# Kernel optimization log

Measured on AMD Instinct MI355X. Metric: run time of the kernel, lower is better.

Reference implementation:

```python
import jax, jax.numpy as jnp
import numpy as np

B, N, D_IN, E, H = 4, 512, 256, 64, 4
NEG = 1.0e9


def setup_inputs() -> dict:
    key = jax.random.key(0)
    ks = jax.random.split(key, 7)
    s = 1.0 / np.sqrt(D_IN)  # dense-init scale
    return {
        "x": jax.random.normal(ks[0], (B, N, D_IN), jnp.float32),
        "Wq": jax.random.normal(ks[1], (H, D_IN, E), jnp.float32) * s,
        "bq": jnp.zeros((H, E), jnp.float32),
        "Wk": jax.random.normal(ks[2], (H, D_IN, E), jnp.float32) * s,
        "bk": jnp.zeros((H, E), jnp.float32),
        "Wv": jax.random.normal(ks[3], (H, D_IN, E), jnp.float32) * s,
        "bv": jnp.zeros((H, E), jnp.float32),
    }


def _sdp(q, k, v):
    logits = jnp.einsum('bne,bme->bnm', q, k) / jnp.sqrt(jnp.asarray(E, q.dtype))
    return jnp.einsum('bnm,bme->bne', jax.nn.softmax(logits, axis=-1), v)


def _cosine(q, k, v):
    qn = q / jnp.linalg.norm(q, axis=-1, keepdims=True)
    kn = k / jnp.linalg.norm(k, axis=-1, keepdims=True)
    logits = jnp.einsum('bne,bme->bnm', qn, kn)
    return jnp.einsum('bnm,bme->bne', jax.nn.softmax(logits, axis=-1), v)


def _l1(q, k, v):
    # [B,N,N] L1 distances via broadcasted [B,N,N,E] diff, as in the original
    d = jnp.sum(jnp.abs(q[:, :, None, :] - k[:, None, :, :]), axis=-1)
    return jnp.einsum('bnm,bme->bne', jax.nn.softmax(-d, axis=-1), v)


def _l2(q, k, v):
    d = jnp.sqrt(jnp.sum(jnp.square(q[:, :, None, :] - k[:, None, :, :]), axis=-1))
    return jnp.einsum('bnm,bme->bne', jax.nn.softmax(-d, axis=-1), v)


_HEAD_FNS = (_sdp, _cosine, _l1, _l2)  # attention_types per head


def reference(x, Wq, bq, Wk, bk, Wv, bv):
    # Per-head projections: [B,H,N,E]
    q = jnp.einsum('bnd,hde->bhne', x, Wq) + bq[None, :, None, :]
    k = jnp.einsum('bnd,hde->bhne', x, Wk) + bk[None, :, None, :]
    v = jnp.einsum('bnd,hde->bhne', x, Wv) + bv[None, :, None, :]
    outs = [fn(q[:, h], k[:, h], v[:, h]) for h, fn in enumerate(_HEAD_FNS)]
    return jnp.concatenate(outs, axis=-1)  # [B,N,H*E]
```

## Files before the change

kernel.cpp:

```cpp
#include <hip/hip_runtime.h>
#include <hip/hip_bf16.h>
#include <math.h>

#define B_   4
#define N_   512
#define DIN  256
#define E_   64
#define H_   4

typedef __attribute__((ext_vector_type(8))) short bf16x8;
typedef __attribute__((ext_vector_type(8))) unsigned short u16x8;
typedef __attribute__((ext_vector_type(4))) float f32x4;

__device__ __forceinline__ unsigned short f2bf(float f) {
    __hip_bfloat16 h = __float2bfloat16(f);
    return *reinterpret_cast<unsigned short*>(&h);
}

__global__ __launch_bounds__(256) void proj_kernel(
    const float* __restrict__ x,
    const float* __restrict__ Wq, const float* __restrict__ bq,
    const float* __restrict__ Wk, const float* __restrict__ bk,
    const float* __restrict__ Wv, const float* __restrict__ bv,
    float* __restrict__ Q, float* __restrict__ KT,
    float* __restrict__ qn2, float* __restrict__ kn2,
    unsigned short* __restrict__ QF, unsigned short* __restrict__ KF,
    unsigned short* __restrict__ VF)
{
    const int tid = threadIdx.x;
    int blk = blockIdx.x;
    const int tile = blk & 15;  blk >>= 4;
    const int p    = blk % 3;   blk /= 3;
    const int h    = blk & 3;
    const int b    = blk >> 2;

    const float* W;
    const float* bias;
    if (p == 0)      { W = Wq; bias = bq; }
    else if (p == 1) { W = Wk; bias = bk; }
    else             { W = Wv; bias = bv; }
    W    += (size_t)h * DIN * E_;
    bias += h * E_;

    const int rowbase = tile * 32;
    const float* xb = x + ((size_t)b * N_ + rowbase) * DIN;

    __shared__ float XsT[64][34];
    __shared__ float Ws[64][64];
    __shared__ float Ys[64][33];
    __shared__ unsigned short Vst[64][48];

    const int tr = tid >> 4;
    const int tc = tid & 15;

    float acc[2][4];
    #pragma unroll
    for (int i = 0; i < 2; ++i)
        #pragma unroll
        for (int j = 0; j < 4; ++j) acc[i][j] = 0.f;

    for (int dc = 0; dc < DIN; dc += 64) {
        for (int l = tid; l < 2048; l += 256) {
            int r = l >> 6, d = l & 63;
            XsT[d][r] = xb[r * DIN + dc + d];
        }
        {
            const float4* Wg4 = (const float4*)(W + (size_t)dc * E_);
            #pragma unroll
            for (int i = 0; i < 4; ++i) ((float4*)Ws)[tid + i * 256] = Wg4[tid + i * 256];
        }
        __syncthreads();

        #pragma unroll 8
        for (int d = 0; d < 64; ++d) {
            float2 xv = *(const float2*)&XsT[d][tr * 2];
            float4 wv = *(const float4*)&Ws[d][tc * 4];
            acc[0][0] = fmaf(xv.x, wv.x, acc[0][0]);
            acc[0][1] = fmaf(xv.x, wv.y, acc[0][1]);
            acc[0][2] = fmaf(xv.x, wv.z, acc[0][2]);
            acc[0][3] = fmaf(xv.x, wv.w, acc[0][3]);
            acc[1][0] = fmaf(xv.y, wv.x, acc[1][0]);
            acc[1][1] = fmaf(xv.y, wv.y, acc[1][1]);
            acc[1][2] = fmaf(xv.y, wv.z, acc[1][2]);
            acc[1][3] = fmaf(xv.y, wv.w, acc[1][3]);
        }
        __syncthreads();
    }

    const size_t bh = (size_t)b * H_ + h;
    float4 bias4 = *(const float4*)&bias[tc * 4];
    float v0[4], v1[4];
    v0[0] = acc[0][0] + bias4.x; v0[1] = acc[0][1] + bias4.y;
    v0[2] = acc[0][2] + bias4.z; v0[3] = acc[0][3] + bias4.w;
    v1[0] = acc[1][0] + bias4.x; v1[1] = acc[1][1] + bias4.y;
    v1[2] = acc[1][2] + bias4.z; v1[3] = acc[1][3] + bias4.w;

    const int r0 = rowbase + tr * 2;

    if (p < 2) {
        float s0 = 0.f, s1 = 0.f;
        #pragma unroll
        for (int j = 0; j < 4; ++j) {
            s0 = fmaf(v0[j], v0[j], s0);
            s1 = fmaf(v1[j], v1[j], s1);
        }
        #pragma unroll
        for (int off = 1; off < 16; off <<= 1) {
            s0 += __shfl_xor(s0, off, 64);
            s1 += __shfl_xor(s1, off, 64);
        }
        if (tc == 0) {
            float* nrm = (p == 0) ? qn2 : kn2;
            nrm[bh * N_ + r0]     = s0;
            nrm[bh * N_ + r0 + 1] = s1;
        }
        unsigned short* f = ((p == 0) ? QF : KF) + bh * (size_t)(N_ * E_);
        const int t_ = r0 >> 4, li = r0 & 15;
        const int gg = tc >> 1, j0 = (tc & 1) * 4;
        ushort4 u0, u1;
        u0.x = f2bf(v0[0]); u0.y = f2bf(v0[1]); u0.z = f2bf(v0[2]); u0.w = f2bf(v0[3]);
        u1.x = f2bf(v1[0]); u1.y = f2bf(v1[1]); u1.z = f2bf(v1[2]); u1.w = f2bf(v1[3]);
        *(ushort4*)&f[(size_t)((t_ * 8 + gg) * 16 + li) * 8 + j0]       = u0;
        *(ushort4*)&f[(size_t)((t_ * 8 + gg) * 16 + li + 1) * 8 + j0]   = u1;
    }

    if (p == 0) {
        float* o = Q + bh * (size_t)(N_ * E_);
        *(float4*)&o[(size_t)r0 * E_ + tc * 4]       = make_float4(v0[0], v0[1], v0[2], v0[3]);
        *(float4*)&o[(size_t)(r0 + 1) * E_ + tc * 4] = make_float4(v1[0], v1[1], v1[2], v1[3]);
    } else if (p == 1) {
        #pragma unroll
        for (int j = 0; j < 4; ++j) {
            Ys[tc * 4 + j][tr * 2]     = v0[j];
            Ys[tc * 4 + j][tr * 2 + 1] = v1[j];
        }
        __syncthreads();
        const int e  = tid >> 2;
        const int n0 = (tid & 3) * 8;
        float* o = KT + bh * (size_t)(E_ * N_) + (size_t)e * N_ + rowbase + n0;
        float4 a, c;
        a.x = Ys[e][n0 + 0]; a.y = Ys[e][n0 + 1];
        a.z = Ys[e][n0 + 2]; a.w = Ys[e][n0 + 3];
        c.x = Ys[e][n0 + 4]; c.y = Ys[e][n0 + 5];
        c.z = Ys[e][n0 + 6]; c.w = Ys[e][n0 + 7];
        *(float4*)&o[0] = a;
        *(float4*)&o[4] = c;
    } else {
        #pragma unroll
        for (int j = 0; j < 4; ++j) {
            Vst[tc * 4 + j][tr * 2]     = f2bf(v0[j]);
            Vst[tc * 4 + j][tr * 2 + 1] = f2bf(v1[j]);
        }
        __syncthreads();
        const int et = tid >> 6, g = (tid >> 4) & 3, li = tid & 15;
        u16x8 wv8 = *(const u16x8*)&Vst[et * 16 + li][g * 8];
        *(u16x8*)&VF[bh * (size_t)(N_ * E_)
                     + (size_t)((((tile * 4 + et) * 4 + g) * 16) + li) * 8] = wv8;
    }
}

template <int HEAD>
__device__ __forceinline__ void mfma_logits32(
    int w, int kh, int lane, size_t bh, int qt, int q0, int pid,
    const unsigned short* __restrict__ QF,
    const unsigned short* __restrict__ KF,
    const float* __restrict__ qn2, const float* __restrict__ kn2,
    char* Pw, float* __restrict__ Mpart, float* __restrict__ Spart)
{
    const int g = lane >> 4, li = lane & 15;
    const int row0 = g * 4;
    const unsigned short* qfb = QF + bh * (N_ * E_) + (size_t)qt * 1024;
    const unsigned short* kfb = KF + bh * (N_ * E_);

    bf16x8 a0 = *(const bf16x8*)&qfb[(g * 16 + li) * 8];
    bf16x8 a1 = *(const bf16x8*)&qfb[((g + 4) * 16 + li) * 8];

    float qrow[4];
    if (HEAD == 1) {
        #pragma unroll
        for (int j = 0; j < 4; ++j) qrow[j] = rsqrtf(qn2[bh * N_ + q0 + row0 + j]);
    } else if (HEAD == 3) {
        #pragma unroll
        for (int j = 0; j < 4; ++j) qrow[j] = qn2[bh * N_ + q0 + row0 + j];
    }

    float lg[2][4];
    #pragma unroll
    for (int t = 0; t < 2; ++t) {
        const int kt = (kh * 4 + w) * 2 + t;
        const int m0 = kt * 16;
        bf16x8 b0 = *(const bf16x8*)&kfb[(size_t)((kt * 8 + g) * 16 + li) * 8];
        bf16x8 b1 = *(const bf16x8*)&kfb[(size_t)((kt * 8 + g + 4) * 16 + li) * 8];
        f32x4 acc = {0.f, 0.f, 0.f, 0.f};
        acc = __builtin_amdgcn_mfma_f32_16x16x32_bf16(a0, b0, acc, 0, 0, 0);
        acc = __builtin_amdgcn_mfma_f32_16x16x32_bf16(a1, b1, acc, 0, 0, 0);
        float kcol = 0.f, rk = 0.f;
        if (HEAD == 1) { kcol = kn2[bh * N_ + m0 + li]; rk = rsqrtf(kcol); }
        if (HEAD == 3) { kcol = kn2[bh * N_ + m0 + li]; }
        #pragma unroll
        for (int j = 0; j < 4; ++j) {
            float d = acc[j];
            if (HEAD == 0)      lg[t][j] = d * 0.125f;
            else if (HEAD == 1) lg[t][j] = d * qrow[j] * rk;
            else                lg[t][j] = -sqrtf(fmaxf(qrow[j] + kcol - 2.f * d, 0.f));
        }
    }

    float mx[4];
    #pragma unroll
    for (int j = 0; j < 4; ++j) {
        float m = fmaxf(lg[0][j], lg[1][j]);
        #pragma unroll
        for (int off = 1; off < 16; off <<= 1) m = fmaxf(m, __shfl_xor(m, off, 64));
        mx[j] = m;
    }

    float sm[4] = {0.f, 0.f, 0.f, 0.f};
    #pragma unroll
    for (int t = 0; t < 2; ++t) {
        #pragma unroll
        for (int j = 0; j < 4; ++j) {
            const int row = row0 + j;
            float pv = __expf(lg[t][j] - mx[j]);
            sm[j] += pv;
            const int byte = (row * 64 + (t * 16 + li) * 2) ^ ((row & 7) << 4);
            *(unsigned short*)(Pw + byte) = f2bf(pv);
        }
    }
    #pragma unroll
    for (int j = 0; j < 4; ++j) {
        float s = sm[j];
        #pragma unroll
        for (int off = 1; off < 16; off <<= 1) s += __shfl_xor(s, off, 64);
        if (li == 0) {
            Mpart[(size_t)pid * 16 + row0 + j] = mx[j];
            Spart[(size_t)pid * 16 + row0 + j] = s;
        }
    }
}

__global__ __launch_bounds__(256) void attn_partial(
    const float* __restrict__ Qf, const float* __restrict__ KT,
    const unsigned short* __restrict__ QF, const unsigned short* __restrict__ KF,
    const unsigned short* __restrict__ VF,
    const float* __restrict__ qn2, const float* __restrict__ kn2,
    float* __restrict__ Opart, float* __restrict__ Mpart,
    float* __restrict__ Spart)
{
    const int tid  = threadIdx.x;
    const int w    = tid >> 6;
    const int lane = tid & 63;
    const int blk  = blockIdx.x;
    const int kh = blk & 3;
    const int qt = (blk >> 2) & 31;
    const int bh = blk >> 7;
    const size_t bhs = (size_t)bh;
    const int q0 = qt * 16;
    const int pid = blk * 4 + w;

    __shared__ unsigned short Plds[4][512];
    __shared__ float q_lds[16][68];

    const int g = lane >> 4, li = lane & 15;
    char* Pw = (char*)&Plds[w][0];
    const int h = bh & 3;

    if (h == 2) {
        {
            const int r = tid >> 4, c0 = (tid & 15) * 4;
            *(float4*)&q_lds[r][c0] =
                *(const float4*)&Qf[bhs * (N_ * E_) + (size_t)(q0 + r) * E_ + c0];
        }
        __syncthreads();

        const int half = lane >> 5;
        const int kloc = lane & 31;
        const int key  = kh * 128 + w * 32 + kloc;
        const float* kp = KT + bhs * (E_ * N_) + key;

        float acc[8];
        #pragma unroll
        for (int i = 0; i < 8; ++i) acc[i] = 0.f;

        #pragma unroll 4
        for (int ec = 0; ec < 16; ++ec) {
            float k0 = kp[(size_t)(ec * 4 + 0) * N_];
            float k1 = kp[(size_t)(ec * 4 + 1) * N_];
            float k2 = kp[(size_t)(ec * 4 + 2) * N_];
            float k3 = kp[(size_t)(ec * 4 + 3) * N_];
            #pragma unroll
            for (int i = 0; i < 8; ++i) {
                float4 q4 = *(const float4*)&q_lds[half * 8 + i][ec * 4];
                acc[i] += fabsf(k0 - q4.x) + fabsf(k1 - q4.y)
                        + fabsf(k2 - q4.z) + fabsf(k3 - q4.w);
            }
        }

        #pragma unroll
        for (int i = 0; i < 8; ++i) {
            const int row = half * 8 + i;
            float mn = acc[i];
            #pragma unroll
            for (int off = 1; off < 32; off <<= 1) mn = fminf(mn, __shfl_xor(mn, off, 64));
            float m = -mn;
            float p = __expf(mn - acc[i]);
            float s = p;
            #pragma unroll
            for (int off = 1; off < 32; off <<= 1) s += __shfl_xor(s, off, 64);
            const int byte = (row * 64 + kloc * 2) ^ ((row & 7) << 4);
            *(unsigned short*)(Pw + byte) = f2bf(p);
            if (kloc == 0) {
                Mpart[(size_t)pid * 16 + row] = m;
                Spart[(size_t)pid * 16 + row] = s;
            }
        }
    } else if (h == 0) {
        mfma_logits32<0>(w, kh, lane, bhs, qt, q0, pid, QF, KF, qn2, kn2, Pw, Mpart, Spart);
    } else if (h == 1) {
        mfma_logits32<1>(w, kh, lane, bhs, qt, q0, pid, QF, KF, qn2, kn2, Pw, Mpart, Spart);
    } else {
        mfma_logits32<3>(w, kh, lane, bhs, qt, q0, pid, QF, KF, qn2, kn2, Pw, Mpart, Spart);
    }
    __syncthreads();

    {
        const int byte = (li * 64 + g * 16) ^ ((li & 7) << 4);
        bf16x8 pa = *(const bf16x8*)(Pw + byte);
        const int kb = kh * 4 + w;
        const unsigned short* vfb = VF + bhs * (N_ * E_);
        #pragma unroll
        for (int et = 0; et < 4; ++et) {
            f32x4 acc = {0.f, 0.f, 0.f, 0.f};
            bf16x8 vb = *(const bf16x8*)&vfb[
                (size_t)((((kb * 4 + et) * 4 + g) * 16) + li) * 8];
            acc = __builtin_amdgcn_mfma_f32_16x16x32_bf16(pa, vb, acc, 0, 0, 0);
            *(f32x4*)&Opart[(size_t)pid * 1024 + ((et * 4 + g) * 16 + li) * 4] = acc;
        }
    }
}

__global__ __launch_bounds__(256) void combine_kernel(
    const float* __restrict__ Opart, const float* __restrict__ Mpart,
    const float* __restrict__ Spart, float* __restrict__ out)
{
    const int tid = threadIdx.x;
    const int blk = blockIdx.x;
    const int qt = blk & 31, bh = blk >> 5;
    const int b = bh >> 2, h = bh & 3;
    const int base = blk * 16;

    __shared__ float ms[16][16], ss[16][16], wls[16][16];
    __shared__ float sginv[16];
    __shared__ float Ot[16][68];

    {
        const int p = tid >> 4, row = tid & 15;
        ms[p][row] = Mpart[(size_t)(base + p) * 16 + row];
        ss[p][row] = Spart[(size_t)(base + p) * 16 + row];
    }
    __syncthreads();
    {
        const int p = tid >> 4, row = tid & 15;
        float mg = ms[0][row];
        #pragma unroll
        for (int q = 1; q < 16; ++q) mg = fmaxf(mg, ms[q][row]);
        wls[p][row] = __expf(ms[p][row] - mg);
    }
    __syncthreads();
    if (tid < 16) {
        float s = 0.f;
        #pragma unroll
        for (int p = 0; p < 16; ++p) s += wls[p][tid] * ss[p][tid];
        sginv[tid] = 1.f / s;
    }
    __syncthreads();

    {
        const int et = tid >> 6, g = (tid >> 4) & 3, li = tid & 15;
        float o0 = 0.f, o1 = 0.f, o2 = 0.f, o3 = 0.f;
        const float* op = Opart + (size_t)base * 1024 + ((et * 4 + g) * 16 + li) * 4;
        #pragma unroll
        for (int p = 0; p < 16; ++p) {
            float4 v = *(const float4*)(op + (size_t)p * 1024);
            o0 = fmaf(wls[p][g * 4 + 0], v.x, o0);
            o1 = fmaf(wls[p][g * 4 + 1], v.y, o1);
            o2 = fmaf(wls[p][g * 4 + 2], v.z, o2);
            o3 = fmaf(wls[p][g * 4 + 3], v.w, o3);
        }
        Ot[g * 4 + 0][et * 16 + li] = o0 * sginv[g * 4 + 0];
        Ot[g * 4 + 1][et * 16 + li] = o1 * sginv[g * 4 + 1];
        Ot[g * 4 + 2][et * 16 + li] = o2 * sginv[g * 4 + 2];
        Ot[g * 4 + 3][et * 16 + li] = o3 * sginv[g * 4 + 3];
    }
    __syncthreads();
    {
        const int row = tid >> 4, e0 = (tid & 15) * 4;
        const int n = qt * 16 + row;
        *(float4*)&out[((size_t)b * N_ + n) * (H_ * E_) + h * E_ + e0] =
            *(const float4*)&Ot[row][e0];
    }
}

extern "C" void kernel_launch(void* const* d_in, const int* in_sizes, int n_in,
                              void* d_out, int out_size, void* d_ws, size_t ws_size,
                              hipStream_t stream)
{
    const float* x  = (const float*)d_in[0];
    const float* Wq = (const float*)d_in[1];
    const float* bq = (const float*)d_in[2];
    const float* Wk = (const float*)d_in[3];
    const float* bk = (const float*)d_in[4];
    const float* Wv = (const float*)d_in[5];
    const float* bv = (const float*)d_in[6];
    float* out = (float*)d_out;

    const size_t qkv = (size_t)B_ * H_ * N_ * E_;
    float* Q     = (float*)d_ws;
    float* KT    = Q + qkv;
    float* qn2   = KT + qkv;
    float* kn2   = qn2 + (size_t)B_ * H_ * N_;
    float* Opart = kn2 + (size_t)B_ * H_ * N_;
    float* Mpart = Opart + (size_t)8192 * 1024;
    float* Spart = Mpart + (size_t)8192 * 16;
    unsigned short* QF = (unsigned short*)(Spart + (size_t)8192 * 16);
    unsigned short* KF = QF + qkv;
    unsigned short* VF = KF + qkv;

    proj_kernel<<<B_ * H_ * 3 * (N_ / 32), 256, 0, stream>>>(
        x, Wq, bq, Wk, bk, Wv, bv, Q, KT, qn2, kn2, QF, KF, VF);
    attn_partial<<<B_ * H_ * 32 * 4, 256, 0, stream>>>(
        Q, KT, QF, KF, VF, qn2, kn2, Opart, Mpart, Spart);
    combine_kernel<<<B_ * H_ * 32, 256, 0, stream>>>(Opart, Mpart, Spart, out);
}
```

Baseline: 53.96 us.

## Drop fp32 Q/K^T copies, read L1 head from bf16 fragments, prefetch K/V

The projection kernel no longer writes fp32 Q and transposed K, and the L1 head now reads its Q and K operands from the bf16 fragment buffers that the MFMA heads already use. This removes the extra global writes and the shared-memory transpose in the projection kernel. The attention kernel also issues its K and V fragment loads up front, before the dependent MFMA and softmax work, so their latency can overlap. The cost is that L1 distances are now computed on bf16-rounded inputs, which lowers their precision.

```diff
diff --git a/kernel.cpp b/kernel.cpp
--- a/kernel.cpp
+++ b/kernel.cpp
@@ -16,13 +16,16 @@
     __hip_bfloat16 h = __float2bfloat16(f);
     return *reinterpret_cast<unsigned short*>(&h);
 }
+__device__ __forceinline__ float bf2f(unsigned short u) {
+    unsigned int v = ((unsigned int)u) << 16;
+    return __uint_as_float(v);
+}
 
 __global__ __launch_bounds__(256) void proj_kernel(
     const float* __restrict__ x,
     const float* __restrict__ Wq, const float* __restrict__ bq,
     const float* __restrict__ Wk, const float* __restrict__ bk,
     const float* __restrict__ Wv, const float* __restrict__ bv,
-    float* __restrict__ Q, float* __restrict__ KT,
     float* __restrict__ qn2, float* __restrict__ kn2,
     unsigned short* __restrict__ QF, unsigned short* __restrict__ KF,
     unsigned short* __restrict__ VF)
@@ -47,7 +50,6 @@
 
     __shared__ float XsT[64][34];
     __shared__ float Ws[64][64];
-    __shared__ float Ys[64][33];
     __shared__ unsigned short Vst[64][48];
 
     const int tr = tid >> 4;
@@ -122,29 +124,6 @@
         u1.x = f2bf(v1[0]); u1.y = f2bf(v1[1]); u1.z = f2bf(v1[2]); u1.w = f2bf(v1[3]);
         *(ushort4*)&f[(size_t)((t_ * 8 + gg) * 16 + li) * 8 + j0]       = u0;
         *(ushort4*)&f[(size_t)((t_ * 8 + gg) * 16 + li + 1) * 8 + j0]   = u1;
-    }
-
-    if (p == 0) {
-        float* o = Q + bh * (size_t)(N_ * E_);
-        *(float4*)&o[(size_t)r0 * E_ + tc * 4]       = make_float4(v0[0], v0[1], v0[2], v0[3]);
-        *(float4*)&o[(size_t)(r0 + 1) * E_ + tc * 4] = make_float4(v1[0], v1[1], v1[2], v1[3]);
-    } else if (p == 1) {
-        #pragma unroll
-        for (int j = 0; j < 4; ++j) {
-            Ys[tc * 4 + j][tr * 2]     = v0[j];
-            Ys[tc * 4 + j][tr * 2 + 1] = v1[j];
-        }
-        __syncthreads();
-        const int e  = tid >> 2;
-        const int n0 = (tid & 3) * 8;
-        float* o = KT + bh * (size_t)(E_ * N_) + (size_t)e * N_ + rowbase + n0;
-        float4 a, c;
-        a.x = Ys[e][n0 + 0]; a.y = Ys[e][n0 + 1];
-        a.z = Ys[e][n0 + 2]; a.w = Ys[e][n0 + 3];
-        c.x = Ys[e][n0 + 4]; c.y = Ys[e][n0 + 5];
-        c.z = Ys[e][n0 + 6]; c.w = Ys[e][n0 + 7];
-        *(float4*)&o[0] = a;
-        *(float4*)&o[4] = c;
     } else {
         #pragma unroll
         for (int j = 0; j < 4; ++j) {
@@ -171,10 +150,19 @@
     const int row0 = g * 4;
     const unsigned short* qfb = QF + bh * (N_ * E_) + (size_t)qt * 1024;
     const unsigned short* kfb = KF + bh * (N_ * E_);
+    const int kt0 = (kh * 4 + w) * 2;
 
     bf16x8 a0 = *(const bf16x8*)&qfb[(g * 16 + li) * 8];
     bf16x8 a1 = *(const bf16x8*)&qfb[((g + 4) * 16 + li) * 8];
-
+    bf16x8 b0a = *(const bf16x8*)&kfb[(size_t)((kt0 * 8 + g) * 16 + li) * 8];
+    bf16x8 b1a = *(const bf16x8*)&kfb[(size_t)((kt0 * 8 + g + 4) * 16 + li) * 8];
+    bf16x8 b0b = *(const bf16x8*)&kfb[(size_t)(((kt0 + 1) * 8 + g) * 16 + li) * 8];
+    bf16x8 b1b = *(const bf16x8*)&kfb[(size_t)(((kt0 + 1) * 8 + g + 4) * 16 + li) * 8];
+    float kc0 = 0.f, kc1 = 0.f;
+    if (HEAD == 1 || HEAD == 3) {
+        kc0 = kn2[bh * N_ + kt0 * 16 + li];
+        kc1 = kn2[bh * N_ + (kt0 + 1) * 16 + li];
+    }
     float qrow[4];
     if (HEAD == 1) {
         #pragma unroll
@@ -184,26 +172,23 @@
         for (int j = 0; j < 4; ++j) qrow[j] = qn2[bh * N_ + q0 + row0 + j];
     }
 
+    f32x4 acca = {0.f, 0.f, 0.f, 0.f};
+    acca = __builtin_amdgcn_mfma_f32_16x16x32_bf16(a0, b0a, acca, 0, 0, 0);
+    acca = __builtin_amdgcn_mfma_f32_16x16x32_bf16(a1, b1a, acca, 0, 0, 0);
+    f32x4 accb = {0.f, 0.f, 0.f, 0.f};
+    accb = __builtin_amdgcn_mfma_f32_16x16x32_bf16(a0, b0b, accb, 0, 0, 0);
+    accb = __builtin_amdgcn_mfma_f32_16x16x32_bf16(a1, b1b, accb, 0, 0, 0);
+
     float lg[2][4];
     #pragma unroll
-    for (int t = 0; t < 2; ++t) {
-        const int kt = (kh * 4 + w) * 2 + t;
-        const int m0 = kt * 16;
-        bf16x8 b0 = *(const bf16x8*)&kfb[(size_t)((kt * 8 + g) * 16 + li) * 8];
-        bf16x8 b1 = *(const bf16x8*)&kfb[(size_t)((kt * 8 + g + 4) * 16 + li) * 8];
-        f32x4 acc = {0.f, 0.f, 0.f, 0.f};
-        acc = __builtin_amdgcn_mfma_f32_16x16x32_bf16(a0, b0, acc, 0, 0, 0);
-        acc = __builtin_amdgcn_mfma_f32_16x16x32_bf16(a1, b1, acc, 0, 0, 0);
-        float kcol = 0.f, rk = 0.f;
-        if (HEAD == 1) { kcol = kn2[bh * N_ + m0 + li]; rk = rsqrtf(kcol); }
-        if (HEAD == 3) { kcol = kn2[bh * N_ + m0 + li]; }
-        #pragma unroll
-        for (int j = 0; j < 4; ++j) {
-            float d = acc[j];
-            if (HEAD == 0)      lg[t][j] = d * 0.125f;
-            else if (HEAD == 1) lg[t][j] = d * qrow[j] * rk;
-            else                lg[t][j] = -sqrtf(fmaxf(qrow[j] + kcol - 2.f * d, 0.f));
-        }
+    for (int j = 0; j < 4; ++j) {
+        float da = acca[j], db = accb[j];
+        if (HEAD == 0)      { lg[0][j] = da * 0.125f; lg[1][j] = db * 0.125f; }
+        else if (HEAD == 1) { float rq = qrow[j];
+                              lg[0][j] = da * rq * rsqrtf(kc0);
+                              lg[1][j] = db * rq * rsqrtf(kc1); }
+        else                { lg[0][j] = -sqrtf(fmaxf(qrow[j] + kc0 - 2.f * da, 0.f));
+                              lg[1][j] = -sqrtf(fmaxf(qrow[j] + kc1 - 2.f * db, 0.f)); }
     }
 
     float mx[4];
@@ -240,7 +225,6 @@
 }
 
 __global__ __launch_bounds__(256) void attn_partial(
-    const float* __restrict__ Qf, const float* __restrict__ KT,
     const unsigned short* __restrict__ QF, const unsigned short* __restrict__ KF,
     const unsigned short* __restrict__ VF,
     const float* __restrict__ qn2, const float* __restrict__ kn2,
@@ -264,35 +248,57 @@
     const int g = lane >> 4, li = lane & 15;
     char* Pw = (char*)&Plds[w][0];
     const int h = bh & 3;
+    const int kb = kh * 4 + w;
+
+    bf16x8 vb[4];
+    {
+        const unsigned short* vfb = VF + bhs * (N_ * E_);
+        #pragma unroll
+        for (int et = 0; et < 4; ++et)
+            vb[et] = *(const bf16x8*)&vfb[(size_t)((((kb * 4 + et) * 4 + g) * 16) + li) * 8];
+    }
 
     if (h == 2) {
-        {
-            const int r = tid >> 4, c0 = (tid & 15) * 4;
-            *(float4*)&q_lds[r][c0] =
-                *(const float4*)&Qf[bhs * (N_ * E_) + (size_t)(q0 + r) * E_ + c0];
-        }
-        __syncthreads();
+        const unsigned short* qfb = QF + bhs * (N_ * E_) + (size_t)qt * 1024;
+        const unsigned short* kfb = KF + bhs * (N_ * E_);
+
+        if (tid < 128) {
+            const int gg = tid >> 4, lr = tid & 15;
+            u16x8 qv = *(const u16x8*)&qfb[(gg * 16 + lr) * 8];
+            #pragma unroll
+            for (int j = 0; j < 8; ++j) q_lds[lr][gg * 8 + j] = bf2f(qv[j]);
+        }
 
         const int half = lane >> 5;
         const int kloc = lane & 31;
         const int key  = kh * 128 + w * 32 + kloc;
-        const float* kp = KT + bhs * (E_ * N_) + key;
+        const int kt = key >> 4, kli = key & 15;
+
+        u16x8 kv[8];
+        #pragma unroll
+        for (int gg = 0; gg < 8; ++gg)
+            kv[gg] = *(const u16x8*)&kfb[(size_t)((kt * 8 + gg) * 16 + kli) * 8];
+
+        __syncthreads();
 
         float acc[8];
         #pragma unroll
         for (int i = 0; i < 8; ++i) acc[i] = 0.f;
 
-        #pragma unroll 4
-        for (int ec = 0; ec < 16; ++ec) {
-            float k0 = kp[(size_t)(ec * 4 + 0) * N_];
-            float k1 = kp[(size_t)(ec * 4 + 1) * N_];
-            float k2 = kp[(size_t)(ec * 4 + 2) * N_];
-            float k3 = kp[(size_t)(ec * 4 + 3) * N_];
+        #pragma unroll
+        for (int gg = 0; gg < 8; ++gg) {
+            float kf[8];
+            #pragma unroll
+            for (int j = 0; j < 8; ++j) kf[j] = bf2f(kv[gg][j]);
             #pragma unroll
             for (int i = 0; i < 8; ++i) {
-                float4 q4 = *(const float4*)&q_lds[half * 8 + i][ec * 4];
-                acc[i] += fabsf(k0 - q4.x) + fabsf(k1 - q4.y)
-                        + fabsf(k2 - q4.z) + fabsf(k3 - q4.w);
+                const float* qr = &q_lds[half * 8 + i][gg * 8];
+                float4 qa = *(const float4*)&qr[0];
+                float4 qc = *(const float4*)&qr[4];
+                acc[i] += fabsf(kf[0] - qa.x) + fabsf(kf[1] - qa.y)
+                        + fabsf(kf[2] - qa.z) + fabsf(kf[3] - qa.w)
+                        + fabsf(kf[4] - qc.x) + fabsf(kf[5] - qc.y)
+                        + fabsf(kf[6] - qc.z) + fabsf(kf[7] - qc.w);
             }
         }
 
@@ -302,7 +308,6 @@
             float mn = acc[i];
             #pragma unroll
             for (int off = 1; off < 32; off <<= 1) mn = fminf(mn, __shfl_xor(mn, off, 64));
-            float m = -mn;
             float p = __expf(mn - acc[i]);
             float s = p;
             #pragma unroll
@@ -310,7 +315,7 @@
             const int byte = (row * 64 + kloc * 2) ^ ((row & 7) << 4);
             *(unsigned short*)(Pw + byte) = f2bf(p);
             if (kloc == 0) {
-                Mpart[(size_t)pid * 16 + row] = m;
+                Mpart[(size_t)pid * 16 + row] = -mn;
                 Spart[(size_t)pid * 16 + row] = s;
             }
         }
@@ -326,14 +331,10 @@
     {
         const int byte = (li * 64 + g * 16) ^ ((li & 7) << 4);
         bf16x8 pa = *(const bf16x8*)(Pw + byte);
-        const int kb = kh * 4 + w;
-        const unsigned short* vfb = VF + bhs * (N_ * E_);
         #pragma unroll
         for (int et = 0; et < 4; ++et) {
             f32x4 acc = {0.f, 0.f, 0.f, 0.f};
-            bf16x8 vb = *(const bf16x8*)&vfb[
-                (size_t)((((kb * 4 + et) * 4 + g) * 16) + li) * 8];
-            acc = __builtin_amdgcn_mfma_f32_16x16x32_bf16(pa, vb, acc, 0, 0, 0);
+            acc = __builtin_amdgcn_mfma_f32_16x16x32_bf16(pa, vb[et], acc, 0, 0, 0);
             *(f32x4*)&Opart[(size_t)pid * 1024 + ((et * 4 + g) * 16 + li) * 4] = acc;
         }
     }
@@ -415,9 +416,7 @@
     float* out = (float*)d_out;
 
     const size_t qkv = (size_t)B_ * H_ * N_ * E_;
-    float* Q     = (float*)d_ws;
-    float* KT    = Q + qkv;
-    float* qn2   = KT + qkv;
+    float* qn2   = (float*)d_ws;
     float* kn2   = qn2 + (size_t)B_ * H_ * N_;
     float* Opart = kn2 + (size_t)B_ * H_ * N_;
     float* Mpart = Opart + (size_t)8192 * 1024;
@@ -427,8 +426,8 @@
     unsigned short* VF = KF + qkv;
 
     proj_kernel<<<B_ * H_ * 3 * (N_ / 32), 256, 0, stream>>>(
-        x, Wq, bq, Wk, bk, Wv, bv, Q, KT, qn2, kn2, QF, KF, VF);
+        x, Wq, bq, Wk, bk, Wv, bv, qn2, kn2, QF, KF, VF);
     attn_partial<<<B_ * H_ * 32 * 4, 256, 0, stream>>>(
-        Q, KT, QF, KF, VF, qn2, kn2, Opart, Mpart, Spart);
+        QF, KF, VF, qn2, kn2, Opart, Mpart, Spart);
     combine_kernel<<<B_ * H_ * 32, 256, 0, stream>>>(Opart, Mpart, Spart, out);
 }
```

Result: slower. 82.46 us (+52.8%).

## Widen per-wave key chunk to 64 and halve attention split-K blocks

Applied to the files above, without the earlier changes.

Each wave now handles 64 keys instead of 32, so the attention kernel launches half as many blocks (2 key splits per query tile instead of 4). The combine kernel merges 8 partials instead of 16, which shrinks the Opart/Mpart/Spart workspace traffic. Per-wave work doubles: more MFMAs per wave, two accumulators in the L1 head, and a larger shared-memory P tile. The cost is less parallelism (2048 blocks down to 1024) and higher register pressure per wave.

```diff
diff --git a/kernel.cpp b/kernel.cpp
--- a/kernel.cpp
+++ b/kernel.cpp
@@ -160,7 +160,7 @@
 }
 
 template <int HEAD>
-__device__ __forceinline__ void mfma_logits32(
+__device__ __forceinline__ void mfma_logits64(
     int w, int kh, int lane, size_t bh, int qt, int q0, int pid,
     const unsigned short* __restrict__ QF,
     const unsigned short* __restrict__ KF,
@@ -171,6 +171,7 @@
     const int row0 = g * 4;
     const unsigned short* qfb = QF + bh * (N_ * E_) + (size_t)qt * 1024;
     const unsigned short* kfb = KF + bh * (N_ * E_);
+    const int kb64 = kh * 4 + w;
 
     bf16x8 a0 = *(const bf16x8*)&qfb[(g * 16 + li) * 8];
     bf16x8 a1 = *(const bf16x8*)&qfb[((g + 4) * 16 + li) * 8];
@@ -184,10 +185,10 @@
         for (int j = 0; j < 4; ++j) qrow[j] = qn2[bh * N_ + q0 + row0 + j];
     }
 
-    float lg[2][4];
+    float lg[4][4];
     #pragma unroll
-    for (int t = 0; t < 2; ++t) {
-        const int kt = (kh * 4 + w) * 2 + t;
+    for (int t = 0; t < 4; ++t) {
+        const int kt = kb64 * 4 + t;
         const int m0 = kt * 16;
         bf16x8 b0 = *(const bf16x8*)&kfb[(size_t)((kt * 8 + g) * 16 + li) * 8];
         bf16x8 b1 = *(const bf16x8*)&kfb[(size_t)((kt * 8 + g + 4) * 16 + li) * 8];
@@ -209,7 +210,7 @@
     float mx[4];
     #pragma unroll
     for (int j = 0; j < 4; ++j) {
-        float m = fmaxf(lg[0][j], lg[1][j]);
+        float m = fmaxf(fmaxf(lg[0][j], lg[1][j]), fmaxf(lg[2][j], lg[3][j]));
         #pragma unroll
         for (int off = 1; off < 16; off <<= 1) m = fmaxf(m, __shfl_xor(m, off, 64));
         mx[j] = m;
@@ -217,13 +218,13 @@
 
     float sm[4] = {0.f, 0.f, 0.f, 0.f};
     #pragma unroll
-    for (int t = 0; t < 2; ++t) {
+    for (int t = 0; t < 4; ++t) {
         #pragma unroll
         for (int j = 0; j < 4; ++j) {
             const int row = row0 + j;
             float pv = __expf(lg[t][j] - mx[j]);
             sm[j] += pv;
-            const int byte = (row * 64 + (t * 16 + li) * 2) ^ ((row & 7) << 4);
+            const int byte = (row * 128 + (t * 16 + li) * 2) ^ ((row & 7) << 4);
             *(unsigned short*)(Pw + byte) = f2bf(pv);
         }
     }
@@ -251,14 +252,15 @@
     const int w    = tid >> 6;
     const int lane = tid & 63;
     const int blk  = blockIdx.x;
-    const int kh = blk & 3;
-    const int qt = (blk >> 2) & 31;
-    const int bh = blk >> 7;
+    const int kh = blk & 1;
+    const int qt = (blk >> 1) & 31;
+    const int bh = blk >> 6;
     const size_t bhs = (size_t)bh;
     const int q0 = qt * 16;
     const int pid = blk * 4 + w;
-
-    __shared__ unsigned short Plds[4][512];
+    const int kb64 = kh * 4 + w;
+
+    __shared__ unsigned short Plds[4][1024];
     __shared__ float q_lds[16][68];
 
     const int g = lane >> 4, li = lane & 15;
@@ -267,73 +269,89 @@
 
     if (h == 2) {
         {
-            const int r = tid >> 4, c0 = (tid & 15) * 4;
-            *(float4*)&q_lds[r][c0] =
-                *(const float4*)&Qf[bhs * (N_ * E_) + (size_t)(q0 + r) * E_ + c0];
+            const int i4 = tid * 4;
+            const int r = i4 >> 6, c = i4 & 63;
+            *(float4*)&q_lds[r][c] =
+                *(const float4*)&Qf[bhs * (N_ * E_) + (size_t)(q0 + r) * E_ + c];
         }
         __syncthreads();
 
         const int half = lane >> 5;
         const int kloc = lane & 31;
-        const int key  = kh * 128 + w * 32 + kloc;
+        const int key  = kb64 * 64 + kloc;
         const float* kp = KT + bhs * (E_ * N_) + key;
 
-        float acc[8];
-        #pragma unroll
-        for (int i = 0; i < 8; ++i) acc[i] = 0.f;
+        float acc0[8], acc1[8];
+        #pragma unroll
+        for (int i = 0; i < 8; ++i) { acc0[i] = 0.f; acc1[i] = 0.f; }
 
         #pragma unroll 4
         for (int ec = 0; ec < 16; ++ec) {
-            float k0 = kp[(size_t)(ec * 4 + 0) * N_];
-            float k1 = kp[(size_t)(ec * 4 + 1) * N_];
-            float k2 = kp[(size_t)(ec * 4 + 2) * N_];
-            float k3 = kp[(size_t)(ec * 4 + 3) * N_];
+            float k00 = kp[(size_t)(ec * 4 + 0) * N_];
+            float k01 = kp[(size_t)(ec * 4 + 0) * N_ + 32];
+            float k10 = kp[(size_t)(ec * 4 + 1) * N_];
+            float k11 = kp[(size_t)(ec * 4 + 1) * N_ + 32];
+            float k20 = kp[(size_t)(ec * 4 + 2) * N_];
+            float k21 = kp[(size_t)(ec * 4 + 2) * N_ + 32];
+            float k30 = kp[(size_t)(ec * 4 + 3) * N_];
+            float k31 = kp[(size_t)(ec * 4 + 3) * N_ + 32];
             #pragma unroll
             for (int i = 0; i < 8; ++i) {
                 float4 q4 = *(const float4*)&q_lds[half * 8 + i][ec * 4];
-                acc[i] += fabsf(k0 - q4.x) + fabsf(k1 - q4.y)
-                        + fabsf(k2 - q4.z) + fabsf(k3 - q4.w);
+                acc0[i] += fabsf(k00 - q4.x) + fabsf(k10 - q4.y)
+                         + fabsf(k20 - q4.z) + fabsf(k30 - q4.w);
+                acc1[i] += fabsf(k01 - q4.x) + fabsf(k11 - q4.y)
+                         + fabsf(k21 - q4.z) + fabsf(k31 - q4.w);
             }
         }
 
         #pragma unroll
         for (int i = 0; i < 8; ++i) {
             const int row = half * 8 + i;
-            float mn = acc[i];
+            float mn = fminf(acc0[i], acc1[i]);
             #pragma unroll
             for (int off = 1; off < 32; off <<= 1) mn = fminf(mn, __shfl_xor(mn, off, 64));
-            float m = -mn;
-            float p = __expf(mn - acc[i]);
-            float s = p;
+            float p0 = __expf(mn - acc0[i]);
+            float p1 = __expf(mn - acc1[i]);
+            float s = p0 + p1;
             #pragma unroll
             for (int off = 1; off < 32; off <<= 1) s += __shfl_xor(s, off, 64);
-            const int byte = (row * 64 + kloc * 2) ^ ((row & 7) << 4);
-            *(unsigned short*)(Pw + byte) = f2bf(p);
+            const int b0 = (row * 128 + kloc * 2) ^ ((row & 7) << 4);
+            const int b1 = (row * 128 + (kloc + 32) * 2) ^ ((row & 7) << 4);
+            *(unsigned short*)(Pw + b0) = f2bf(p0);
+            *(unsigned short*)(Pw + b1) = f2bf(p1);
             if (kloc == 0) {
-                Mpart[(size_t)pid * 16 + row] = m;
+                Mpart[(size_t)pid * 16 + row] = -mn;
                 Spart[(size_t)pid * 16 + row] = s;
             }
         }
     } else if (h == 0) {
-        mfma_logits32<0>(w, kh, lane, bhs, qt, q0, pid, QF, KF, qn2, kn2, Pw, Mpart, Spart);
+        mfma_logits64<0>(w, kh, lane, bhs, qt, q0, pid, QF, KF, qn2, kn2, Pw, Mpart, Spart);
     } else if (h == 1) {
-        mfma_logits32<1>(w, kh, lane, bhs, qt, q0, pid, QF, KF, qn2, kn2, Pw, Mpart, Spart);
+        mfma_logits64<1>(w, kh, lane, bhs, qt, q0, pid, QF, KF, qn2, kn2, Pw, Mpart, Spart);
     } else {
-        mfma_logits32<3>(w, kh, lane, bhs, qt, q0, pid, QF, KF, qn2, kn2, Pw, Mpart, Spart);
+        mfma_logits64<3>(w, kh, lane, bhs, qt, q0, pid, QF, KF, qn2, kn2, Pw, Mpart, Spart);
     }
     __syncthreads();
 
     {
-        const int byte = (li * 64 + g * 16) ^ ((li & 7) << 4);
-        bf16x8 pa = *(const bf16x8*)(Pw + byte);
-        const int kb = kh * 4 + w;
+        bf16x8 pa[2];
+        #pragma unroll
+        for (int s = 0; s < 2; ++s) {
+            const int byte = (li * 128 + (s * 32 + g * 8) * 2) ^ ((li & 7) << 4);
+            pa[s] = *(const bf16x8*)(Pw + byte);
+        }
         const unsigned short* vfb = VF + bhs * (N_ * E_);
         #pragma unroll
         for (int et = 0; et < 4; ++et) {
             f32x4 acc = {0.f, 0.f, 0.f, 0.f};
-            bf16x8 vb = *(const bf16x8*)&vfb[
-                (size_t)((((kb * 4 + et) * 4 + g) * 16) + li) * 8];
-            acc = __builtin_amdgcn_mfma_f32_16x16x32_bf16(pa, vb, acc, 0, 0, 0);
+            #pragma unroll
+            for (int s = 0; s < 2; ++s) {
+                const int kb32 = kb64 * 2 + s;
+                bf16x8 vb = *(const bf16x8*)&vfb[
+                    (size_t)((((kb32 * 4 + et) * 4 + g) * 16) + li) * 8];
+                acc = __builtin_amdgcn_mfma_f32_16x16x32_bf16(pa[s], vb, acc, 0, 0, 0);
+            }
             *(f32x4*)&Opart[(size_t)pid * 1024 + ((et * 4 + g) * 16 + li) * 4] = acc;
         }
     }
@@ -347,30 +365,30 @@
     const int blk = blockIdx.x;
     const int qt = blk & 31, bh = blk >> 5;
     const int b = bh >> 2, h = bh & 3;
-    const int base = blk * 16;
-
-    __shared__ float ms[16][16], ss[16][16], wls[16][16];
+    const int base = blk * 8;
+
+    __shared__ float ms[8][16], ss[8][16], wls[8][16];
     __shared__ float sginv[16];
     __shared__ float Ot[16][68];
 
-    {
+    if (tid < 128) {
         const int p = tid >> 4, row = tid & 15;
         ms[p][row] = Mpart[(size_t)(base + p) * 16 + row];
         ss[p][row] = Spart[(size_t)(base + p) * 16 + row];
     }
     __syncthreads();
-    {
+    if (tid < 128) {
         const int p = tid >> 4, row = tid & 15;
         float mg = ms[0][row];
         #pragma unroll
-        for (int q = 1; q < 16; ++q) mg = fmaxf(mg, ms[q][row]);
+        for (int q = 1; q < 8; ++q) mg = fmaxf(mg, ms[q][row]);
         wls[p][row] = __expf(ms[p][row] - mg);
     }
     __syncthreads();
     if (tid < 16) {
         float s = 0.f;
         #pragma unroll
-        for (int p = 0; p < 16; ++p) s += wls[p][tid] * ss[p][tid];
+        for (int p = 0; p < 8; ++p) s += wls[p][tid] * ss[p][tid];
         sginv[tid] = 1.f / s;
     }
     __syncthreads();
@@ -380,7 +398,7 @@
         float o0 = 0.f, o1 = 0.f, o2 = 0.f, o3 = 0.f;
         const float* op = Opart + (size_t)base * 1024 + ((et * 4 + g) * 16 + li) * 4;
         #pragma unroll
-        for (int p = 0; p < 16; ++p) {
+        for (int p = 0; p < 8; ++p) {
             float4 v = *(const float4*)(op + (size_t)p * 1024);
             o0 = fmaf(wls[p][g * 4 + 0], v.x, o0);
             o1 = fmaf(wls[p][g * 4 + 1], v.y, o1);
@@ -420,15 +438,15 @@
     float* qn2   = KT + qkv;
     float* kn2   = qn2 + (size_t)B_ * H_ * N_;
     float* Opart = kn2 + (size_t)B_ * H_ * N_;
-    float* Mpart = Opart + (size_t)8192 * 1024;
-    float* Spart = Mpart + (size_t)8192 * 16;
-    unsigned short* QF = (unsigned short*)(Spart + (size_t)8192 * 16);
+    float* Mpart = Opart + (size_t)4096 * 1024;
+    float* Spart = Mpart + (size_t)4096 * 16;
+    unsigned short* QF = (unsigned short*)(Spart + (size_t)4096 * 16);
     unsigned short* KF = QF + qkv;
     unsigned short* VF = KF + qkv;
 
     proj_kernel<<<B_ * H_ * 3 * (N_ / 32), 256, 0, stream>>>(
         x, Wq, bq, Wk, bk, Wv, bv, Q, KT, qn2, kn2, QF, KF, VF);
-    attn_partial<<<B_ * H_ * 32 * 4, 256, 0, stream>>>(
+    attn_partial<<<B_ * H_ * 32 * 2, 256, 0, stream>>>(
         Q, KT, QF, KF, VF, qn2, kn2, Opart, Mpart, Spart);
     combine_kernel<<<B_ * H_ * 32, 256, 0, stream>>>(Opart, Mpart, Spart, out);
 }
```

Result: slower. 59.62 us (+10.5%).
